# Kernel tuning notes

Measured on AMD Instinct MI355X. Metric: run time of the kernel, lower is better.

## Reference

```python
import jax, jax.numpy as jnp
import numpy as np

DIM = 768
HEADS = 12


def setup_inputs() -> dict:
    key = jax.random.key(0)
    k1, k2, k3, k4 = jax.random.split(key, 4)
    x = jax.random.normal(k1, (8, 1024, DIM), dtype=jnp.float32)
    # qkv: Linear(dim, 3*dim, bias=False); torch stores weight as (out, in), y = x @ W.T
    w_qkv = jax.random.normal(k2, (3 * DIM, DIM), dtype=jnp.float32) * (DIM ** -0.5)
    w_fc = jax.random.normal(k3, (DIM, DIM), dtype=jnp.float32) * (DIM ** -0.5)
    b_fc = jax.random.normal(k4, (DIM,), dtype=jnp.float32) * 0.02
    return {"x": x, "w_qkv": w_qkv, "w_fc": w_fc, "b_fc": b_fc}


def reference(x, w_qkv, w_fc, b_fc):
    b, n, dim = x.shape
    h = HEADS
    d = dim // h
    qkv = jnp.einsum('bnd,ed->bne', x, w_qkv)  # [b, n, 3*dim]
    q, k, v = jnp.split(qkv, 3, axis=-1)
    # b n (h d) -> b h n d
    q = q.reshape(b, n, h, d).transpose(0, 2, 1, 3)
    k = k.reshape(b, n, h, d).transpose(0, 2, 1, 3)
    v = v.reshape(b, n, h, d).transpose(0, 2, 1, 3)
    # NOTE: original module computes d_k = dim**-0.5 but never applies it.
    scores = jnp.einsum('bhqd,bhkd->bhqk', q, k)  # unscaled, faithful to source
    attn = jax.nn.softmax(scores, axis=-1)
    out = jnp.einsum('bhqk,bhkd->bhqd', attn, v)
    out = out.transpose(0, 2, 1, 3).reshape(b, n, dim)  # b h n d -> b n (h d)
    out = jnp.einsum('bnd,ed->bne', out, w_fc) + b_fc
    return out
```

## Files before the change

### kernel.cpp

```cpp
#include <hip/hip_runtime.h>
#include <cstdint>
#include <cstddef>

typedef __bf16 bf16;
typedef __bf16 bf16x4 __attribute__((ext_vector_type(4)));
typedef __bf16 bf16x8 __attribute__((ext_vector_type(8)));
typedef float f32x4 __attribute__((ext_vector_type(4)));
typedef float f32x16 __attribute__((ext_vector_type(16)));

typedef const __attribute__((address_space(1))) void* gas_ptr;
typedef __attribute__((address_space(3))) void* las_ptr;

#define GLOAD_LDS16(g, l) __builtin_amdgcn_global_load_lds((gas_ptr)(g), (las_ptr)(l), 16, 0, 0)

__global__ void cvt_f32_bf16(const float* __restrict__ in, bf16* __restrict__ out, int n4) {
  int i = blockIdx.x * blockDim.x + threadIdx.x;
  int stride = gridDim.x * blockDim.x;
  for (; i < n4; i += stride) {
    float4 v = reinterpret_cast<const float4*>(in)[i];
    bf16x4 o;
    o[0] = (bf16)v.x; o[1] = (bf16)v.y; o[2] = (bf16)v.z; o[3] = (bf16)v.w;
    reinterpret_cast<bf16x4*>(out)[i] = o;
  }
}

template <int MODE>
__global__ __launch_bounds__(512, 4) void gemm_bt(
    const bf16* __restrict__ A, const bf16* __restrict__ B,
    int M, int N, int K,
    bf16* __restrict__ outb, float* __restrict__ outf,
    const float* __restrict__ bias) {
  constexpr int BK = 32;
  __shared__ bf16 lds[3][12288];
  const int tid = threadIdx.x;
  const int l = tid & 63;
  const int w = tid >> 6;
  const int wr = w >> 1, wc = w & 1;
  const int lr = l & 15, lg = l >> 4;

  const int bid = blockIdx.y * 32 + blockIdx.x;
  const int xcd = bid & 7, c = bid >> 3;
  const int brow = (xcd * 4 + (c & 3)) * 256;
  const int bcol = (c >> 2) * 128;

  const bf16* sa0 = A + (size_t)(brow + w * 16 + lr) * K + lg * 8;
  const bf16* sa1 = sa0 + (size_t)128 * K;
  const bf16* sb0 = B + (size_t)(bcol + w * 16 + lr) * K + lg * 8;
  const int dA0 = w * 512 + l * 8;
  const int dA1 = (8 + w) * 512 + l * 8;
  const int dB0 = 8192 + w * 512 + l * 8;

  f32x4 acc[4][4] = {};

  GLOAD_LDS16(sa0, &lds[0][dA0]);
  GLOAD_LDS16(sa1, &lds[0][dA1]);
  GLOAD_LDS16(sb0, &lds[0][dB0]);
  GLOAD_LDS16(sa0 + BK, &lds[1][dA0]);
  GLOAD_LDS16(sa1 + BK, &lds[1][dA1]);
  GLOAD_LDS16(sb0 + BK, &lds[1][dB0]);

  int p = 0;
  for (int k0 = 0; k0 < K; k0 += BK) {
    asm volatile("s_waitcnt vmcnt(3)" ::: "memory");
    __builtin_amdgcn_sched_barrier(0);
    __builtin_amdgcn_s_barrier();
    __builtin_amdgcn_sched_barrier(0);

    int kn = k0 + 2 * BK;
    if (kn >= K) kn = k0;
    const int pt = (p >= 1) ? p - 1 : 2;
    GLOAD_LDS16(sa0 + kn, &lds[pt][dA0]);
    GLOAD_LDS16(sa1 + kn, &lds[pt][dA1]);
    GLOAD_LDS16(sb0 + kn, &lds[pt][dB0]);

    bf16x8 af[4], bfr[4];
#pragma unroll
    for (int mi = 0; mi < 4; mi++)
      af[mi] = *reinterpret_cast<const bf16x8*>(&lds[p][(wr * 4 + mi) * 512 + l * 8]);
#pragma unroll
    for (int ni = 0; ni < 4; ni++)
      bfr[ni] = *reinterpret_cast<const bf16x8*>(&lds[p][8192 + (wc * 4 + ni) * 512 + l * 8]);
#pragma unroll
    for (int mi = 0; mi < 4; mi++)
#pragma unroll
      for (int ni = 0; ni < 4; ni++)
        acc[mi][ni] = __builtin_amdgcn_mfma_f32_16x16x32_bf16(af[mi], bfr[ni], acc[mi][ni], 0, 0, 0);
    p = (p == 2) ? 0 : p + 1;
  }

#pragma unroll
  for (int mi = 0; mi < 4; mi++) {
#pragma unroll
    for (int r = 0; r < 4; r++) {
      const int m = brow + wr * 64 + mi * 16 + lg * 4 + r;
#pragma unroll
      for (int ni = 0; ni < 4; ni++) {
        const int e = bcol + wc * 64 + ni * 16 + lr;
        const float v = acc[mi][ni][r];
        if (MODE == 1) {
          outf[(size_t)m * N + e] = v + bias[e];
        } else {
          outb[(size_t)m * N + e] = (bf16)v;
        }
      }
    }
  }
}

__global__ __launch_bounds__(256) void vtrans(const bf16* __restrict__ qkv,
                                              bf16* __restrict__ vtb) {
  __shared__ bf16 t[64 * 72];
  const int bh = blockIdx.x;
  const int b = bh / 12, h = bh % 12;
  const int nt = blockIdx.y;
  const int tid = threadIdx.x;
#pragma unroll
  for (int it = 0; it < 2; it++) {
    const int item = tid + it * 256;
    const int nl = item >> 3, c = item & 7;
    bf16x8 v = *reinterpret_cast<const bf16x8*>(
        &qkv[(size_t)(b * 1024 + nt * 64 + nl) * 2304 + 1536 + h * 64 + c * 8]);
#pragma unroll
    for (int j = 0; j < 8; j++) t[(c * 8 + j) * 72 + nl] = v[j];
  }
  __syncthreads();
#pragma unroll
  for (int it = 0; it < 2; it++) {
    const int item = tid + it * 256;
    const int d = item >> 3, c2 = item & 7;
    bf16x8 v = *reinterpret_cast<const bf16x8*>(&t[d * 72 + c2 * 8]);
    *reinterpret_cast<bf16x8*>(
        &vtb[(size_t)bh * 65536 + d * 1024 + nt * 64 + c2 * 8]) = v;
  }
}

__global__ __launch_bounds__(256, 3) void attn_kernel(
    const bf16* __restrict__ QKV, const bf16* __restrict__ Vt,
    bf16* __restrict__ Out) {
  __shared__ bf16 Kb[2][4096];
  __shared__ bf16 Vb[2][4096];
  const int tid = threadIdx.x;
  const int l = tid & 63;
  const int w = tid >> 6;
  const int ql = l & 31;
  const int hi = l >> 5;
  const int bh = blockIdx.x;
  const int b = bh / 12, h = bh % 12;
  const int q0 = blockIdx.y * 128 + w * 32;
  const bf16* Vh = Vt + (size_t)bh * 65536;
  constexpr float L2E = 1.4426950408889634f;

  const int kdst0 = (0 * 4 + w) * 512 + l * 8;
  const int kdst1 = (1 * 4 + w) * 512 + l * 8;
  const bf16* ksrc0 = QKV + (size_t)(b * 1024 + ql) * 2304 + 768 + h * 64 + w * 16 + hi * 8;
  const bf16* ksrc1 = ksrc0 + (size_t)32 * 2304;
  const bf16* vsrc0 = Vh + (size_t)((w & 1) * 32 + ql) * 1024 + ((0 * 4 + w) >> 1) * 16 + hi * 8;
  const bf16* vsrc1 = Vh + (size_t)((w & 1) * 32 + ql) * 1024 + ((1 * 4 + w) >> 1) * 16 + hi * 8;

  const bf16* Qrow = QKV + (size_t)(b * 1024 + q0 + ql) * 2304 + h * 64;
  bf16x8 qf[4];
#pragma unroll
  for (int s = 0; s < 4; s++)
    qf[s] = *reinterpret_cast<const bf16x8*>(&Qrow[s * 16 + hi * 8]);

  f32x16 o[2] = {};
  float ls0 = 0.f, ls1 = 0.f, ls2 = 0.f, ls3 = 0.f;

  GLOAD_LDS16(ksrc0, &Kb[0][kdst0]);
  GLOAD_LDS16(ksrc1, &Kb[0][kdst1]);
  GLOAD_LDS16(vsrc0, &Vb[0][kdst0]);
  GLOAD_LDS16(vsrc1, &Vb[0][kdst1]);
  asm volatile("s_waitcnt vmcnt(0)" ::: "memory");
  __syncthreads();

  int p = 0;
  for (int it = 0; it < 16; ++it) {
    const int kt = it * 64;
    if (it < 15) {
      GLOAD_LDS16(ksrc0 + (size_t)(kt + 64) * 2304, &Kb[p ^ 1][kdst0]);
      GLOAD_LDS16(ksrc1 + (size_t)(kt + 64) * 2304, &Kb[p ^ 1][kdst1]);
      GLOAD_LDS16(vsrc0 + (kt + 64), &Vb[p ^ 1][kdst0]);
      GLOAD_LDS16(vsrc1 + (kt + 64), &Vb[p ^ 1][kdst1]);
    }

    bf16x8 kf[8];
#pragma unroll
    for (int r = 0; r < 8; r++)
      kf[r] = *reinterpret_cast<const bf16x8*>(&Kb[p][r * 512 + l * 8]);
    f32x16 st0 = {}, st1 = {};
    __builtin_amdgcn_s_setprio(1);
#pragma unroll
    for (int s = 0; s < 4; s++) {
      st0 = __builtin_amdgcn_mfma_f32_32x32x16_bf16(kf[s], qf[s], st0, 0, 0, 0);
      st1 = __builtin_amdgcn_mfma_f32_32x32x16_bf16(kf[4 + s], qf[s], st1, 0, 0, 0);
    }
    __builtin_amdgcn_s_setprio(0);

#pragma unroll
    for (int r = 0; r < 16; r++) {
      float a0 = st0[r] * L2E, a1 = st1[r] * L2E;
      float e0, e1;
      asm("v_exp_f32 %0, %1" : "=v"(e0) : "v"(a0));
      asm("v_exp_f32 %0, %1" : "=v"(e1) : "v"(a1));
      st0[r] = e0; st1[r] = e1;
    }
#pragma unroll
    for (int r = 0; r < 16; r += 2) {
      ls0 += st0[r]; ls1 += st0[r + 1];
      ls2 += st1[r]; ls3 += st1[r + 1];
    }

    bf16x8 pfv[4];
#pragma unroll
    for (int t = 0; t < 4; t++) {
      const int c8 = (t & 1) * 8;
      const f32x16& sv = (t < 2) ? st0 : st1;
      uint32_t wA0, wA1, wB0, wB1;
      asm("v_cvt_pk_bf16_f32 %0, %1, %2" : "=v"(wA0) : "v"(sv[c8 + 0]), "v"(sv[c8 + 1]));
      asm("v_cvt_pk_bf16_f32 %0, %1, %2" : "=v"(wA1) : "v"(sv[c8 + 2]), "v"(sv[c8 + 3]));
      asm("v_cvt_pk_bf16_f32 %0, %1, %2" : "=v"(wB0) : "v"(sv[c8 + 4]), "v"(sv[c8 + 5]));
      asm("v_cvt_pk_bf16_f32 %0, %1, %2" : "=v"(wB1) : "v"(sv[c8 + 6]), "v"(sv[c8 + 7]));
      asm("v_permlane32_swap_b32 %0, %1" : "+v"(wA0), "+v"(wB0));
      asm("v_permlane32_swap_b32 %0, %1" : "+v"(wA1), "+v"(wB1));
      union { uint32_t u[4]; bf16x8 v; } pf;
      pf.u[0] = wA0; pf.u[1] = wA1; pf.u[2] = wB0; pf.u[3] = wB1;
      pfv[t] = pf.v;
    }

    bf16x8 vf[8];
#pragma unroll
    for (int r = 0; r < 8; r++)
      vf[r] = *reinterpret_cast<const bf16x8*>(&Vb[p][r * 512 + l * 8]);
    __builtin_amdgcn_s_setprio(1);
#pragma unroll
    for (int t = 0; t < 4; t++) {
      o[0] = __builtin_amdgcn_mfma_f32_32x32x16_bf16(vf[t * 2 + 0], pfv[t], o[0], 0, 0, 0);
      o[1] = __builtin_amdgcn_mfma_f32_32x32x16_bf16(vf[t * 2 + 1], pfv[t], o[1], 0, 0, 0);
    }
    __builtin_amdgcn_s_setprio(0);

    asm volatile("s_waitcnt vmcnt(0)" ::: "memory");
    __syncthreads();
    p ^= 1;
  }

  float lsum = (ls0 + ls1) + (ls2 + ls3);
  lsum += __shfl_xor(lsum, 32);
  const float rl = 1.0f / lsum;
  bf16* orow = Out + (size_t)(b * 1024 + q0 + ql) * 768 + h * 64;
#pragma unroll
  for (int dh = 0; dh < 2; dh++)
#pragma unroll
    for (int rq = 0; rq < 4; rq++) {
      union { ushort us[4]; uint2 v; } pk;
#pragma unroll
      for (int i = 0; i < 4; i++) {
        const bf16 hv = (bf16)(o[dh][rq * 4 + i] * rl);
        pk.us[i] = __builtin_bit_cast(ushort, hv);
      }
      *reinterpret_cast<uint2*>(&orow[dh * 32 + rq * 8 + hi * 4]) = pk.v;
    }
}

extern "C" void kernel_launch(void* const* d_in, const int* in_sizes, int n_in,
                              void* d_out, int out_size, void* d_ws, size_t ws_size,
                              hipStream_t stream) {
  const float* x = (const float*)d_in[0];
  const float* w_qkv = (const float*)d_in[1];
  const float* w_fc = (const float*)d_in[2];
  const float* b_fc = (const float*)d_in[3];
  float* out = (float*)d_out;
  char* ws = (char*)d_ws;

  bf16* xb = (bf16*)(ws);
  bf16* vtb = (bf16*)(ws);
  bf16* wqkb = (bf16*)(ws + 12582912);
  bf16* wfcb = (bf16*)(ws + 16121856);
  bf16* qkvb = (bf16*)(ws + 17301504);
  bf16* aob = (bf16*)(ws + 55050240);

  cvt_f32_bf16<<<2048, 256, 0, stream>>>(x, xb, 6291456 / 4);
  cvt_f32_bf16<<<1728, 256, 0, stream>>>(w_qkv, wqkb, 1769472 / 4);
  cvt_f32_bf16<<<576, 256, 0, stream>>>(w_fc, wfcb, 589824 / 4);

  gemm_bt<0><<<dim3(32, 18), 512, 0, stream>>>(xb, wqkb, 8192, 2304, 768,
                                               qkvb, nullptr, nullptr);

  vtrans<<<dim3(96, 16), 256, 0, stream>>>(qkvb, vtb);

  attn_kernel<<<dim3(96, 8), 256, 0, stream>>>(qkvb, vtb, aob);

  gemm_bt<1><<<dim3(32, 6), 512, 0, stream>>>(aob, wfcb, 8192, 768, 768,
                                              nullptr, out, b_fc);
}
```

Measured before the change: 145.0 us.

## Add 256x256-tile QKV GEMM kernel with double-buffered direct-to-LDS loads

Replaces the QKV projection GEMM with a new kernel that computes 256x256 output tiles per 512-thread block, using BK=64 double-buffered global_load_lds staging interleaved across four MFMA sub-phases. The larger tile raises arithmetic intensity and cuts global/LDS traffic per FLOP compared to the previous gemm_bt tiling. In exchange it uses 128KB of LDS and many accumulator registers, which lowers occupancy. The grid also shrinks to 288 blocks, which may leave some compute units idle.

```diff
diff --git a/kernel.cpp b/kernel.cpp
--- a/kernel.cpp
+++ b/kernel.cpp
@@ -22,6 +22,145 @@
     o[0] = (bf16)v.x; o[1] = (bf16)v.y; o[2] = (bf16)v.z; o[3] = (bf16)v.w;
     reinterpret_cast<bf16x4*>(out)[i] = o;
   }
+}
+
+__global__ __launch_bounds__(512, 2) void gemm256(
+    const bf16* __restrict__ A, const bf16* __restrict__ B,
+    int M, int N, int K, bf16* __restrict__ outb) {
+  __shared__ bf16 lds[2][32768];
+  const int tid = threadIdx.x;
+  const int l = tid & 63;
+  const int w = tid >> 6;
+  const int wr = w >> 2, wc = w & 3;
+  const int lr = l & 15, lg = l >> 4;
+
+  const int bid = blockIdx.y * gridDim.x + blockIdx.x;
+  const int xcd = bid & 7, c = bid >> 3;
+  const int brow = (xcd * 4 + (c & 3)) * 256;
+  const int bcol = (c >> 2) * 256;
+
+  const bf16* asrc[4];
+  const bf16* bsrc[4];
+  int adst[4], bdst[4];
+#pragma unroll
+  for (int t = 0; t < 4; t++) {
+    const int ai = w * 4 + t, kh = ai >> 4, s = ai & 15;
+    asrc[t] = A + (size_t)(brow + s * 16 + lr) * K + kh * 32 + lg * 8;
+    bsrc[t] = B + (size_t)(bcol + s * 16 + lr) * K + kh * 32 + lg * 8;
+    adst[t] = kh * 8192 + s * 512 + l * 8;
+    bdst[t] = 16384 + kh * 8192 + s * 512 + l * 8;
+  }
+
+  f32x4 acc[8][4] = {};
+
+#pragma unroll
+  for (int t = 0; t < 4; t++) {
+    GLOAD_LDS16(asrc[t], &lds[0][adst[t]]);
+    GLOAD_LDS16(bsrc[t], &lds[0][bdst[t]]);
+  }
+
+  const int NS = K >> 6;
+  int p = 0;
+  for (int step = 0; step < NS; step++) {
+    const int k0 = step << 6;
+    const int kn = (step + 1 < NS) ? k0 + 64 : k0;
+    asm volatile("s_waitcnt vmcnt(0)" ::: "memory");
+    __builtin_amdgcn_sched_barrier(0);
+    __builtin_amdgcn_s_barrier();
+    __builtin_amdgcn_sched_barrier(0);
+    const int q = p ^ 1;
+    bf16x8 bfr[4];
+
+    {
+      bf16x8 af[4];
+#pragma unroll
+      for (int j = 0; j < 4; j++)
+        bfr[j] = *reinterpret_cast<const bf16x8*>(&lds[p][16384 + (wc * 4 + j) * 512 + l * 8]);
+#pragma unroll
+      for (int i = 0; i < 4; i++)
+        af[i] = *reinterpret_cast<const bf16x8*>(&lds[p][(wr * 8 + i) * 512 + l * 8]);
+      GLOAD_LDS16(asrc[0] + kn, &lds[q][adst[0]]);
+      GLOAD_LDS16(asrc[1] + kn, &lds[q][adst[1]]);
+      GLOAD_LDS16(bsrc[0] + kn, &lds[q][bdst[0]]);
+      __builtin_amdgcn_sched_barrier(0);
+      __builtin_amdgcn_s_setprio(1);
+#pragma unroll
+      for (int i = 0; i < 4; i++)
+#pragma unroll
+        for (int j = 0; j < 4; j++)
+          acc[i][j] = __builtin_amdgcn_mfma_f32_16x16x32_bf16(af[i], bfr[j], acc[i][j], 0, 0, 0);
+      __builtin_amdgcn_s_setprio(0);
+      __builtin_amdgcn_sched_barrier(0);
+      __builtin_amdgcn_s_barrier();
+    }
+    {
+      bf16x8 af[4];
+#pragma unroll
+      for (int i = 0; i < 4; i++)
+        af[i] = *reinterpret_cast<const bf16x8*>(&lds[p][(wr * 8 + 4 + i) * 512 + l * 8]);
+      GLOAD_LDS16(asrc[2] + kn, &lds[q][adst[2]]);
+      GLOAD_LDS16(asrc[3] + kn, &lds[q][adst[3]]);
+      GLOAD_LDS16(bsrc[1] + kn, &lds[q][bdst[1]]);
+      __builtin_amdgcn_sched_barrier(0);
+      __builtin_amdgcn_s_setprio(1);
+#pragma unroll
+      for (int i = 0; i < 4; i++)
+#pragma unroll
+        for (int j = 0; j < 4; j++)
+          acc[4 + i][j] = __builtin_amdgcn_mfma_f32_16x16x32_bf16(af[i], bfr[j], acc[4 + i][j], 0, 0, 0);
+      __builtin_amdgcn_s_setprio(0);
+      __builtin_amdgcn_sched_barrier(0);
+      __builtin_amdgcn_s_barrier();
+    }
+    {
+      bf16x8 af[4];
+#pragma unroll
+      for (int j = 0; j < 4; j++)
+        bfr[j] = *reinterpret_cast<const bf16x8*>(&lds[p][16384 + 8192 + (wc * 4 + j) * 512 + l * 8]);
+#pragma unroll
+      for (int i = 0; i < 4; i++)
+        af[i] = *reinterpret_cast<const bf16x8*>(&lds[p][8192 + (wr * 8 + i) * 512 + l * 8]);
+      GLOAD_LDS16(bsrc[2] + kn, &lds[q][bdst[2]]);
+      GLOAD_LDS16(bsrc[3] + kn, &lds[q][bdst[3]]);
+      __builtin_amdgcn_sched_barrier(0);
+      __builtin_amdgcn_s_setprio(1);
+#pragma unroll
+      for (int i = 0; i < 4; i++)
+#pragma unroll
+        for (int j = 0; j < 4; j++)
+          acc[i][j] = __builtin_amdgcn_mfma_f32_16x16x32_bf16(af[i], bfr[j], acc[i][j], 0, 0, 0);
+      __builtin_amdgcn_s_setprio(0);
+      __builtin_amdgcn_sched_barrier(0);
+      __builtin_amdgcn_s_barrier();
+    }
+    {
+      bf16x8 af[4];
+#pragma unroll
+      for (int i = 0; i < 4; i++)
+        af[i] = *reinterpret_cast<const bf16x8*>(&lds[p][8192 + (wr * 8 + 4 + i) * 512 + l * 8]);
+      __builtin_amdgcn_sched_barrier(0);
+      __builtin_amdgcn_s_setprio(1);
+#pragma unroll
+      for (int i = 0; i < 4; i++)
+#pragma unroll
+        for (int j = 0; j < 4; j++)
+          acc[4 + i][j] = __builtin_amdgcn_mfma_f32_16x16x32_bf16(af[i], bfr[j], acc[4 + i][j], 0, 0, 0);
+      __builtin_amdgcn_s_setprio(0);
+    }
+    p = q;
+  }
+
+#pragma unroll
+  for (int si = 0; si < 8; si++)
+#pragma unroll
+    for (int r = 0; r < 4; r++) {
+      const int m = brow + (wr * 8 + si) * 16 + lg * 4 + r;
+#pragma unroll
+      for (int j = 0; j < 4; j++) {
+        const int e = bcol + (wc * 4 + j) * 16 + lr;
+        outb[(size_t)m * N + e] = (bf16)acc[si][j][r];
+      }
+    }
 }
 
 template <int MODE>
@@ -283,8 +422,7 @@
   cvt_f32_bf16<<<1728, 256, 0, stream>>>(w_qkv, wqkb, 1769472 / 4);
   cvt_f32_bf16<<<576, 256, 0, stream>>>(w_fc, wfcb, 589824 / 4);
 
-  gemm_bt<0><<<dim3(32, 18), 512, 0, stream>>>(xb, wqkb, 8192, 2304, 768,
-                                               qkvb, nullptr, nullptr);
+  gemm256<<<dim3(32, 9), 512, 0, stream>>>(xb, wqkb, 8192, 2304, 768, qkvb);
 
   vtrans<<<dim3(96, 16), 256, 0, stream>>>(qkvb, vtb);
 
```

New measurement: 150.9 us. 1.04x slower.
